# Kernel tuning notes

Hardware: AMD Instinct MI355X
Metric: run time of the kernel (lower is better)

Reference implementation:

```python
import jax, jax.numpy as jnp
import numpy as np
from jax import lax

H = 1024
E = 8
TOP_K = 2


def setup_inputs() -> dict:
    key = jax.random.key(0)
    kx, k1, k2 = jax.random.split(key, 3)
    x = jax.random.normal(kx, (8, 2048, H), dtype=jnp.float32)
    # router MLP params, init normal(0, 0.02), zero bias (matches _init_weights)
    w1 = jax.random.normal(k1, (H, 2 * H), dtype=jnp.float32) * 0.02
    b1 = jnp.zeros((2 * H,), dtype=jnp.float32)
    w2 = jax.random.normal(k2, (2 * H, E), dtype=jnp.float32) * 0.02
    b2 = jnp.zeros((E,), dtype=jnp.float32)
    return {"x": x, "w1": w1, "b1": b1, "w2": w2, "b2": b2}


def reference(x, w1, b1, w2, b2):
    # gating MLP: Linear -> GELU (exact, torch default) -> Linear
    h = jax.nn.gelu(jnp.einsum('bsh,hf->bsf', x, w1) + b1, approximate=False)
    expert_weights = jnp.einsum('bsf,fe->bse', h, w2) + b2  # [B,S,E]

    top_k_weights, top_k_indices = lax.top_k(expert_weights, TOP_K)  # [B,S,K]
    top_k_weights = jax.nn.softmax(top_k_weights, axis=-1)

    # scatter renormalized weights into dense [B,S,E] mask (indices distinct -> one-hot sum)
    onehot = jax.nn.one_hot(top_k_indices, E, dtype=expert_weights.dtype)  # [B,S,K,E]
    masks = jnp.einsum('bsk,bske->bse', top_k_weights, onehot)

    expert_usage = masks.sum(axis=(0, 1))
    expert_usage = expert_usage / expert_usage.sum()
    target_usage = jnp.full_like(expert_usage, 1.0 / E)
    load_balancing_loss = jnp.mean((expert_usage - target_usage) ** 2)

    sparsity_loss = jnp.mean(jnp.sum(masks > 0, axis=-1).astype(jnp.float32)) / TOP_K
    total_loss = load_balancing_loss + 0.1 * sparsity_loss

    return expert_weights, masks, total_loss, expert_usage
```

## Files before the change

kernel.cpp:

```cpp
#include <hip/hip_runtime.h>
#include <math.h>

#define HDIM 1024
#define FDIM 2048
#define NEXP 8
#define MTOK 16384
#define NSLC 32

#define ROWS 2048

typedef __attribute__((ext_vector_type(8))) short bf16x8;
typedef __attribute__((ext_vector_type(4))) float f32x4;

__device__ inline unsigned short f2bf_rne(float f) {
    unsigned int u = __float_as_uint(f);
    u = (u + 0x7FFFu + ((u >> 16) & 1u)) >> 16;
    return (unsigned short)u;
}
__device__ inline float bf2f(unsigned short h) {
    unsigned int u = ((unsigned int)h) << 16;
    return __uint_as_float(u);
}

__global__ __launch_bounds__(256) void cvt_x(const float* __restrict__ x,
                                             unsigned short* __restrict__ xi)
{
    size_t g = (size_t)blockIdx.x * 256 + threadIdx.x;
    size_t m = g >> 7, k8 = g & 127;
    const float* p = x + g * 8;
    float v[8];
    *(float4*)(v)     = *(const float4*)(p);
    *(float4*)(v + 4) = *(const float4*)(p + 4);
    union { unsigned short u[8]; uint4 q; } oh, ol;
    #pragma unroll
    for (int j = 0; j < 8; j++) {
        unsigned short h = f2bf_rne(v[j]);
        oh.u[j] = h;
        ol.u[j] = f2bf_rne(v[j] - bf2f(h));
    }
    unsigned short* dst = xi + m * ROWS + k8 * 16;
    *(uint4*)dst = oh.q;
    *(uint4*)(dst + 8) = ol.q;
}

__global__ __launch_bounds__(256) void cvt_w1t(const float* __restrict__ w1,
                                               unsigned short* __restrict__ wi)
{
    __shared__ float t[32][33];
    int n0 = blockIdx.x * 32;
    int k0 = blockIdx.y * 32;
    int lx = threadIdx.x & 31, ly = threadIdx.x >> 5;
    #pragma unroll
    for (int r = 0; r < 32; r += 8)
        t[ly + r][lx] = w1[(size_t)(k0 + ly + r) * FDIM + n0 + lx];
    __syncthreads();
    #pragma unroll
    for (int r = 0; r < 32; r += 8) {
        float v = t[lx][ly + r];
        unsigned short h = f2bf_rne(v);
        unsigned short l = f2bf_rne(v - bf2f(h));
        int k = k0 + lx;
        size_t o = (size_t)(n0 + ly + r) * ROWS + (size_t)(k >> 3) * 16 + (k & 7);
        wi[o] = h;
        wi[o + 8] = l;
    }
}

#define BM 128
#define BN 128

__global__ __launch_bounds__(256, 2) void gemm1_mfma(
    const unsigned short* __restrict__ xi, const unsigned short* __restrict__ wi,
    const float* __restrict__ b1, const float* __restrict__ w2,
    float* __restrict__ part)
{
    __shared__ __align__(16) short As[2][BM * 64];
    __shared__ __align__(16) short Bs[2][BN * 64];

    const int tid  = threadIdx.x;
    const int lane = tid & 63;
    const int l15  = lane & 15;
    const int q    = lane >> 4;
    const int wave = tid >> 6;
    const int wm   = wave & 1;
    const int wn   = wave >> 1;
    const int bn = blockIdx.x, bm = blockIdx.y;
    const int m0 = bm * BM, n0 = bn * BN;

    const unsigned short* ap[4];
    const unsigned short* bp[4];
    #pragma unroll
    for (int s = 0; s < 4; s++) {
        int cc = s * 256 + tid;
        int m = cc >> 3;
        int j = (cc & 7) ^ (m & 7);
        ap[s] = xi + (size_t)(m0 + m) * ROWS + j * 8;
        bp[s] = wi + (size_t)(n0 + m) * ROWS + j * 8;
    }

    int offA[2][4], offB[2][4];
    #pragma unroll
    for (int i = 0; i < 4; i++) {
        int ma = wm * 64 + i * 16 + l15;
        offA[0][i] = (ma * 8 + ((2 * q)     ^ (ma & 7))) * 8;
        offA[1][i] = (ma * 8 + ((2 * q + 1) ^ (ma & 7))) * 8;
        int nb = wn * 64 + i * 16 + l15;
        offB[0][i] = (nb * 8 + ((2 * q)     ^ (nb & 7))) * 8;
        offB[1][i] = (nb * 8 + ((2 * q + 1) ^ (nb & 7))) * 8;
    }

    f32x4 acc[4][4];
    #pragma unroll
    for (int i = 0; i < 4; i++)
        #pragma unroll
        for (int j = 0; j < 4; j++) acc[i][j] = (f32x4){0.f, 0.f, 0.f, 0.f};

    #pragma unroll
    for (int s = 0; s < 4; s++) {
        int lo = (s * 256 + tid) * 8;
        __builtin_amdgcn_global_load_lds(
            (const __attribute__((address_space(1))) void*)(ap[s]),
            (__attribute__((address_space(3))) void*)&As[0][lo], 16, 0, 0);
        __builtin_amdgcn_global_load_lds(
            (const __attribute__((address_space(1))) void*)(bp[s]),
            (__attribute__((address_space(3))) void*)&Bs[0][lo], 16, 0, 0);
    }

    for (int t = 0; t < 32; t++) {
        __syncthreads();
        if (t + 1 < 32) {
            const int nbuf = (t + 1) & 1;
            #pragma unroll
            for (int s = 0; s < 4; s++) {
                int lo = (s * 256 + tid) * 8;
                __builtin_amdgcn_global_load_lds(
                    (const __attribute__((address_space(1))) void*)(ap[s] + (t + 1) * 64),
                    (__attribute__((address_space(3))) void*)&As[nbuf][lo], 16, 0, 0);
                __builtin_amdgcn_global_load_lds(
                    (const __attribute__((address_space(1))) void*)(bp[s] + (t + 1) * 64),
                    (__attribute__((address_space(3))) void*)&Bs[nbuf][lo], 16, 0, 0);
            }
        }
        const short* a = As[t & 1];
        const short* b = Bs[t & 1];

        bf16x8 ah[4], al[4], bh[4], bl[4];
        #pragma unroll
        for (int i = 0; i < 4; i++) {
            ah[i] = *(const bf16x8*)&a[offA[0][i]];
            al[i] = *(const bf16x8*)&a[offA[1][i]];
            bh[i] = *(const bf16x8*)&b[offB[0][i]];
            bl[i] = *(const bf16x8*)&b[offB[1][i]];
        }
        #pragma unroll
        for (int i = 0; i < 4; i++)
            #pragma unroll
            for (int j = 0; j < 4; j++) {
                acc[i][j] = __builtin_amdgcn_mfma_f32_16x16x32_bf16(
                    ah[i], bh[j], acc[i][j], 0, 0, 0);
                acc[i][j] = __builtin_amdgcn_mfma_f32_16x16x32_bf16(
                    ah[i], bl[j], acc[i][j], 0, 0, 0);
                acc[i][j] = __builtin_amdgcn_mfma_f32_16x16x32_bf16(
                    al[i], bh[j], acc[i][j], 0, 0, 0);
            }
    }

    #pragma unroll
    for (int j = 0; j < 4; j++) {
        int n = n0 + wn * 64 + j * 16 + l15;
        float bb = b1[n];
        #pragma unroll
        for (int i = 0; i < 4; i++)
            #pragma unroll
            for (int r = 0; r < 4; r++) {
                float v = acc[i][j][r] + bb;
                acc[i][j][r] = 0.5f * v * (1.0f + erff(v * 0.70710678118654752f));
            }
    }

    float w2r[4][8];
    #pragma unroll
    for (int j = 0; j < 4; j++) {
        const float4* p = (const float4*)(w2 + (size_t)(n0 + wn * 64 + j * 16 + l15) * NEXP);
        float4 u = p[0], v = p[1];
        w2r[j][0] = u.x; w2r[j][1] = u.y; w2r[j][2] = u.z; w2r[j][3] = u.w;
        w2r[j][4] = v.x; w2r[j][5] = v.y; w2r[j][6] = v.z; w2r[j][7] = v.w;
    }

    const int sl = bn * 2 + wn;
    #pragma unroll
    for (int e = 0; e < NEXP; e++) {
        float p[4][4];
        #pragma unroll
        for (int i = 0; i < 4; i++)
            #pragma unroll
            for (int r = 0; r < 4; r++) {
                float s = 0.f;
                #pragma unroll
                for (int j = 0; j < 4; j++) s += acc[i][j][r] * w2r[j][e];
                p[i][r] = s;
            }
        #pragma unroll
        for (int off = 1; off < 16; off <<= 1)
            #pragma unroll
            for (int i = 0; i < 4; i++)
                #pragma unroll
                for (int r = 0; r < 4; r++)
                    p[i][r] += __shfl_xor(p[i][r], off);
        if (l15 == 0) {
            #pragma unroll
            for (int i = 0; i < 4; i++)
                #pragma unroll
                for (int r = 0; r < 4; r++) {
                    int m = m0 + wm * 64 + i * 16 + q * 4 + r;
                    part[(size_t)sl * (MTOK * NEXP) + (size_t)m * NEXP + e] = p[i][r];
                }
        }
    }
}

__global__ __launch_bounds__(256) void router_topk(
    const float* __restrict__ part, const float* __restrict__ b2,
    float* __restrict__ out, float* __restrict__ gu, int* __restrict__ gc)
{
    const int t = blockIdx.x * 256 + threadIdx.x;

    float logit[8];
    #pragma unroll
    for (int e = 0; e < 8; e++) logit[e] = b2[e];
    #pragma unroll
    for (int j = 0; j < NSLC; j++) {
        const float4* p4 = (const float4*)(part + (size_t)j * (MTOK * NEXP) + (size_t)t * NEXP);
        float4 u = p4[0], v = p4[1];
        logit[0] += u.x; logit[1] += u.y; logit[2] += u.z; logit[3] += u.w;
        logit[4] += v.x; logit[5] += v.y; logit[6] += v.z; logit[7] += v.w;
    }

    int i1 = 0; float v1 = logit[0];
    #pragma unroll
    for (int e = 1; e < 8; e++) { if (logit[e] > v1) { v1 = logit[e]; i1 = e; } }
    int i2 = -1; float v2 = -INFINITY;
    #pragma unroll
    for (int e = 0; e < 8; e++) {
        if (e != i1 && logit[e] > v2) { v2 = logit[e]; i2 = e; }
    }
    float ex = expf(v2 - v1);
    float inv = 1.0f / (1.0f + ex);
    float wa = inv, wb = ex * inv;

    float4* o = (float4*)(out + (size_t)t * NEXP);
    o[0] = make_float4(logit[0], logit[1], logit[2], logit[3]);
    o[1] = make_float4(logit[4], logit[5], logit[6], logit[7]);

    float mk[8];
    #pragma unroll
    for (int e = 0; e < 8; e++) mk[e] = 0.0f;
    mk[i1] = wa; mk[i2] = wb;
    float4* om = (float4*)(out + (size_t)(MTOK * NEXP) + (size_t)t * NEXP);
    om[0] = make_float4(mk[0], mk[1], mk[2], mk[3]);
    om[1] = make_float4(mk[4], mk[5], mk[6], mk[7]);

    __shared__ float us[8];
    __shared__ int cs;
    if (threadIdx.x < 8) us[threadIdx.x] = 0.0f;
    if (threadIdx.x == 0) cs = 0;
    __syncthreads();
    atomicAdd(&us[i1], wa);
    atomicAdd(&us[i2], wb);
    int cnt = (wa > 0.0f ? 1 : 0) + (wb > 0.0f ? 1 : 0);
    atomicAdd(&cs, cnt);
    __syncthreads();
    if (threadIdx.x < 8) atomicAdd(&gu[threadIdx.x], us[threadIdx.x]);
    if (threadIdx.x == 0) atomicAdd(gc, cs);
}

__global__ void router_final(const float* __restrict__ gu, const int* __restrict__ gc,
                             float* __restrict__ out)
{
    if (blockIdx.x == 0 && threadIdx.x == 0) {
        float u[8]; float tot = 0.0f;
        for (int e = 0; e < 8; e++) { u[e] = gu[e]; tot += u[e]; }
        float lb = 0.0f;
        for (int e = 0; e < 8; e++) {
            float un = u[e] / tot;
            out[2 * MTOK * NEXP + 1 + e] = un;
            float d = un - 0.125f;
            lb += d * d;
        }
        lb *= (1.0f / 8.0f);
        float sp = ((float)(*gc) / (float)MTOK) * 0.5f;
        out[2 * MTOK * NEXP] = lb + 0.1f * sp;
    }
}

extern "C" void kernel_launch(void* const* d_in, const int* in_sizes, int n_in,
                              void* d_out, int out_size, void* d_ws, size_t ws_size,
                              hipStream_t stream) {
    const float* x  = (const float*)d_in[0];
    const float* w1 = (const float*)d_in[1];
    const float* b1 = (const float*)d_in[2];
    const float* w2 = (const float*)d_in[3];
    const float* b2 = (const float*)d_in[4];
    float* out = (float*)d_out;

    unsigned short* xi = (unsigned short*)d_ws;
    unsigned short* wi = xi + (size_t)MTOK * ROWS;
    float* part = (float*)(wi + (size_t)FDIM * ROWS);
    float* gu = part + (size_t)NSLC * MTOK * NEXP;
    int* gc = (int*)(gu + 8);

    hipMemsetAsync(gu, 0, 64, stream);

    cvt_x<<<(MTOK * HDIM / 8) / 256, 256, 0, stream>>>(x, xi);
    cvt_w1t<<<dim3(FDIM / 32, HDIM / 32), 256, 0, stream>>>(w1, wi);
    gemm1_mfma<<<dim3(FDIM / BN, MTOK / BM), 256, 0, stream>>>(xi, wi, b1, w2, part);
    router_topk<<<MTOK / 256, 256, 0, stream>>>(part, b2, out, gu, gc);
    router_final<<<1, 64, 0, stream>>>(gu, gc, out);
}
```

Baseline: 363.2 us.

## Pre-swizzle W1 into MFMA fragment layout and load B directly to registers

The W1 conversion kernel now writes the hi/lo bf16 weights in a per-16-column, per-32-k fragment order, so each lane can load its MFMA B operand straight from global memory with one 16-byte read. The B tile no longer goes through LDS, which halves LDS traffic and footprint in the GEMM. The grid is also transposed so consecutive blocks share the same weight columns. In exchange, B loads are issued synchronously at the top of each k-step with no prefetch, so their global/L2 latency is exposed unless occupancy hides it.

```diff
diff --git a/kernel.cpp b/kernel.cpp
--- a/kernel.cpp
+++ b/kernel.cpp
@@ -6,8 +6,9 @@
 #define NEXP 8
 #define MTOK 16384
 #define NSLC 32
-
 #define ROWS 2048
+#define BM 128
+#define BN 128
 
 typedef __attribute__((ext_vector_type(8))) short bf16x8;
 typedef __attribute__((ext_vector_type(4))) float f32x4;
@@ -43,8 +44,8 @@
     *(uint4*)(dst + 8) = ol.q;
 }
 
-__global__ __launch_bounds__(256) void cvt_w1t(const float* __restrict__ w1,
-                                               unsigned short* __restrict__ wi)
+__global__ __launch_bounds__(256) void cvt_w1f(const float* __restrict__ w1,
+                                               unsigned short* __restrict__ wf)
 {
     __shared__ float t[32][33];
     int n0 = blockIdx.x * 32;
@@ -59,23 +60,20 @@
         float v = t[lx][ly + r];
         unsigned short h = f2bf_rne(v);
         unsigned short l = f2bf_rne(v - bf2f(h));
-        int k = k0 + lx;
-        size_t o = (size_t)(n0 + ly + r) * ROWS + (size_t)(k >> 3) * 16 + (k & 7);
-        wi[o] = h;
-        wi[o + 8] = l;
-    }
-}
-
-#define BM 128
-#define BN 128
+        int n = n0 + ly + r, k = k0 + lx;
+        size_t base = (size_t)((n >> 4) * 32 + (k >> 5)) * 1024;
+        int lj = (((k >> 3) & 3) * 16 + (n & 15)) * 8 + (k & 7);
+        wf[base + lj] = h;
+        wf[base + 512 + lj] = l;
+    }
+}
 
 __global__ __launch_bounds__(256, 2) void gemm1_mfma(
-    const unsigned short* __restrict__ xi, const unsigned short* __restrict__ wi,
+    const unsigned short* __restrict__ xi, const unsigned short* __restrict__ wf,
     const float* __restrict__ b1, const float* __restrict__ w2,
     float* __restrict__ part)
 {
     __shared__ __align__(16) short As[2][BM * 64];
-    __shared__ __align__(16) short Bs[2][BN * 64];
 
     const int tid  = threadIdx.x;
     const int lane = tid & 63;
@@ -84,29 +82,33 @@
     const int wave = tid >> 6;
     const int wm   = wave & 1;
     const int wn   = wave >> 1;
-    const int bn = blockIdx.x, bm = blockIdx.y;
+    const int bm = blockIdx.x, bn = blockIdx.y;
     const int m0 = bm * BM, n0 = bn * BN;
 
     const unsigned short* ap[4];
-    const unsigned short* bp[4];
     #pragma unroll
     for (int s = 0; s < 4; s++) {
-        int cc = s * 256 + tid;
-        int m = cc >> 3;
-        int j = (cc & 7) ^ (m & 7);
-        ap[s] = xi + (size_t)(m0 + m) * ROWS + j * 8;
-        bp[s] = wi + (size_t)(n0 + m) * ROWS + j * 8;
-    }
-
-    int offA[2][4], offB[2][4];
+        int c = s * 256 + tid;
+        int m = c >> 3;
+        int g = (c & 7) ^ (m & 7);
+        ap[s] = xi + (size_t)(m0 + m) * ROWS + g * 8;
+    }
+
+    const unsigned short* bq[4][2];
+    #pragma unroll
+    for (int f = 0; f < 4; f++) {
+        int nt = bn * 8 + wn * 4 + f;
+        #pragma unroll
+        for (int h = 0; h < 2; h++)
+            bq[f][h] = wf + (size_t)nt * 32768 + h * 512 + lane * 8;
+    }
+
+    int offA[2][4];
     #pragma unroll
     for (int i = 0; i < 4; i++) {
         int ma = wm * 64 + i * 16 + l15;
         offA[0][i] = (ma * 8 + ((2 * q)     ^ (ma & 7))) * 8;
         offA[1][i] = (ma * 8 + ((2 * q + 1) ^ (ma & 7))) * 8;
-        int nb = wn * 64 + i * 16 + l15;
-        offB[0][i] = (nb * 8 + ((2 * q)     ^ (nb & 7))) * 8;
-        offB[1][i] = (nb * 8 + ((2 * q + 1) ^ (nb & 7))) * 8;
     }
 
     f32x4 acc[4][4];
@@ -116,41 +118,37 @@
         for (int j = 0; j < 4; j++) acc[i][j] = (f32x4){0.f, 0.f, 0.f, 0.f};
 
     #pragma unroll
-    for (int s = 0; s < 4; s++) {
-        int lo = (s * 256 + tid) * 8;
+    for (int s = 0; s < 4; s++)
         __builtin_amdgcn_global_load_lds(
             (const __attribute__((address_space(1))) void*)(ap[s]),
-            (__attribute__((address_space(3))) void*)&As[0][lo], 16, 0, 0);
-        __builtin_amdgcn_global_load_lds(
-            (const __attribute__((address_space(1))) void*)(bp[s]),
-            (__attribute__((address_space(3))) void*)&Bs[0][lo], 16, 0, 0);
-    }
+            (__attribute__((address_space(3))) void*)&As[0][(s * 256 + tid) * 8],
+            16, 0, 0);
 
     for (int t = 0; t < 32; t++) {
         __syncthreads();
+
+        bf16x8 bh[4], bl[4];
+        #pragma unroll
+        for (int f = 0; f < 4; f++) {
+            bh[f] = *(const bf16x8*)(bq[f][0] + t * 1024);
+            bl[f] = *(const bf16x8*)(bq[f][1] + t * 1024);
+        }
         if (t + 1 < 32) {
             const int nbuf = (t + 1) & 1;
             #pragma unroll
-            for (int s = 0; s < 4; s++) {
-                int lo = (s * 256 + tid) * 8;
+            for (int s = 0; s < 4; s++)
                 __builtin_amdgcn_global_load_lds(
                     (const __attribute__((address_space(1))) void*)(ap[s] + (t + 1) * 64),
-                    (__attribute__((address_space(3))) void*)&As[nbuf][lo], 16, 0, 0);
-                __builtin_amdgcn_global_load_lds(
-                    (const __attribute__((address_space(1))) void*)(bp[s] + (t + 1) * 64),
-                    (__attribute__((address_space(3))) void*)&Bs[nbuf][lo], 16, 0, 0);
-            }
-        }
+                    (__attribute__((address_space(3))) void*)&As[nbuf][(s * 256 + tid) * 8],
+                    16, 0, 0);
+        }
+
         const short* a = As[t & 1];
-        const short* b = Bs[t & 1];
-
-        bf16x8 ah[4], al[4], bh[4], bl[4];
+        bf16x8 ah[4], al[4];
         #pragma unroll
         for (int i = 0; i < 4; i++) {
             ah[i] = *(const bf16x8*)&a[offA[0][i]];
             al[i] = *(const bf16x8*)&a[offA[1][i]];
-            bh[i] = *(const bf16x8*)&b[offB[0][i]];
-            bl[i] = *(const bf16x8*)&b[offB[1][i]];
         }
         #pragma unroll
         for (int i = 0; i < 4; i++)
@@ -304,16 +302,16 @@
     float* out = (float*)d_out;
 
     unsigned short* xi = (unsigned short*)d_ws;
-    unsigned short* wi = xi + (size_t)MTOK * ROWS;
-    float* part = (float*)(wi + (size_t)FDIM * ROWS);
+    unsigned short* wf = xi + (size_t)MTOK * ROWS;
+    float* part = (float*)(wf + (size_t)128 * 32 * 1024);
     float* gu = part + (size_t)NSLC * MTOK * NEXP;
     int* gc = (int*)(gu + 8);
 
     hipMemsetAsync(gu, 0, 64, stream);
 
     cvt_x<<<(MTOK * HDIM / 8) / 256, 256, 0, stream>>>(x, xi);
-    cvt_w1t<<<dim3(FDIM / 32, HDIM / 32), 256, 0, stream>>>(w1, wi);
-    gemm1_mfma<<<dim3(FDIM / BN, MTOK / BM), 256, 0, stream>>>(xi, wi, b1, w2, part);
+    cvt_w1f<<<dim3(FDIM / 32, HDIM / 32), 256, 0, stream>>>(w1, wf);
+    gemm1_mfma<<<dim3(MTOK / BM, FDIM / BN), 256, 0, stream>>>(xi, wf, b1, w2, part);
     router_topk<<<MTOK / 256, 256, 0, stream>>>(part, b2, out, gu, gc);
     router_final<<<1, 64, 0, stream>>>(gu, gc, out);
 }
```

Result: faster. 351.6 us (-3.2%).
